# Performance work log

Hardware: AMD Instinct MI355X
Metric: run time of the kernel (lower is better)

The kernel has to match this reference:

```python
import jax, jax.numpy as jnp
import numpy as np
from jax import lax

IN_CH = 512
OUT_CH = 512
K = 3
W_DIM = 512
PAD = K // 2
EPS = 1e-8


def setup_inputs() -> dict:
    key = jax.random.key(0)
    k1, k2, k3, k4 = jax.random.split(key, 4)
    B, H, W = 8, 64, 64
    x = jax.random.normal(k1, (B, IN_CH, H, W), dtype=jnp.float32)
    w = jax.random.normal(k2, (B, W_DIM), dtype=jnp.float32)
    weight = jax.random.normal(k3, (OUT_CH, IN_CH, K, K), dtype=jnp.float32)
    bias = jnp.zeros((OUT_CH,), dtype=jnp.float32)
    # nn.Linear(512, in_ch): weight [in_ch, 512], bias [in_ch]
    lim = 1.0 / np.sqrt(W_DIM)
    affine_w = jax.random.uniform(k4, (IN_CH, W_DIM), dtype=jnp.float32, minval=-lim, maxval=lim)
    affine_b = jnp.zeros((IN_CH,), dtype=jnp.float32)
    return {"x": x, "w": w, "weight": weight, "bias": bias,
            "affine_w": affine_w, "affine_b": affine_b}


def _conv_one(xi, wi):
    # xi: [C, H, W], wi: [O, C, K, K] -> [O, H, W]
    out = lax.conv_general_dilated(
        xi[None], wi, window_strides=(1, 1),
        padding=[(PAD, PAD), (PAD, PAD)],
        dimension_numbers=("NCHW", "OIHW", "NCHW"))
    return out[0]


def reference(x, w, weight, bias, affine_w, affine_b):
    # style: [B, C] -> broadcast as [B, 1, C, 1, 1]
    style = w @ affine_w.T + affine_b
    wmod = weight[None] * (style[:, None, :, None, None] + 1.0)  # [B, O, C, K, K]
    # demodulate
    sigma = lax.rsqrt(jnp.sum(wmod * wmod, axis=(2, 3, 4), keepdims=True) + EPS)
    wmod = wmod * sigma
    # per-sample conv (equivalent to groups=B grouped conv)
    out = jax.vmap(_conv_one)(x, wmod)  # [B, O, H, W]
    return out + bias[None, :, None, None]
```

## Files before the change

kernel.cpp:

```cpp
#include <hip/hip_runtime.h>
#include <hip/hip_bf16.h>

typedef __attribute__((ext_vector_type(8))) short bf16x8;
typedef __attribute__((ext_vector_type(4))) float f32x4;

#define FSW(c) (((c) >> 1) & 3)

static __device__ __forceinline__ uint bf16rne(float f) {
    uint u = __float_as_uint(f);
    return (u + 0x7fffu + ((u >> 16) & 1u)) >> 16;
}

__global__ void k_style(const float* __restrict__ w, const float* __restrict__ aw,
                        const float* __restrict__ ab, float* __restrict__ style) {
    int idx = blockIdx.x * 4 + (threadIdx.x >> 6);
    int lane = threadIdx.x & 63;
    int b = idx >> 9, c = idx & 511;
    const float* wp = w + b * 512;
    const float* ap = aw + (size_t)c * 512;
    float s = 0.f;
    #pragma unroll
    for (int i = 0; i < 8; ++i) s += wp[lane + i * 64] * ap[lane + i * 64];
    #pragma unroll
    for (int m = 32; m; m >>= 1) s += __shfl_xor(s, m, 64);
    if (lane == 0) style[idx] = s + ab[c] + 1.0f;
}

__global__ void k_wprep(const float* __restrict__ weight, ushort* __restrict__ Wf,
                        float* __restrict__ wsq) {
    int t = blockIdx.x * 256 + threadIdx.x;
    int o = t >> 9, c = t & 511;
    int grp = o >> 5, rr = o & 31, fm = rr >> 4, l15r = rr & 15;
    int chunkid = c >> 5, kgw = (c >> 3) & 3, kk = c & 7;
    int lanew = kgw * 16 + l15r;
    const float* wp = weight + (size_t)t * 9;
    size_t G = (size_t)(grp * 16 + chunkid);
    size_t base = G * 9216 + (size_t)fm * 512 + (size_t)lanew * 8 + kk;
    float sq = 0.f;
    #pragma unroll
    for (int j = 0; j < 9; ++j) {
        float v = wp[j];
        sq += v * v;
        Wf[base + (size_t)j * 1024] = (ushort)bf16rne(v);
    }
    wsq[t] = sq;
}

__global__ void k_sigma(const float* __restrict__ style, const float* __restrict__ wsq,
                        float* __restrict__ sigma) {
    int idx = blockIdx.x * 4 + (threadIdx.x >> 6);
    int lane = threadIdx.x & 63;
    int b = idx >> 9, o = idx & 511;
    const float* sp = style + b * 512;
    const float* qp = wsq + (size_t)o * 512;
    float s = 0.f;
    #pragma unroll
    for (int i = 0; i < 8; ++i) {
        float st = sp[lane + i * 64];
        s += st * st * qp[lane + i * 64];
    }
    #pragma unroll
    for (int m = 32; m; m >>= 1) s += __shfl_xor(s, m, 64);
    if (lane == 0) sigma[idx] = rsqrtf(s + 1e-8f);
}

__global__ void k_premod(const float* __restrict__ x, const float* __restrict__ style,
                         ushort* __restrict__ xb) {
    int bid = blockIdx.x;
    int b = bid >> 6, y = bid & 63;
    int xcol = threadIdx.x >> 2, cg = threadIdx.x & 3;
    const float* sp = style + b * 512;
    #pragma unroll 1
    for (int cb = 0; cb < 16; ++cb) {
        int c0 = cb * 32 + cg * 8;
        float v[8];
        #pragma unroll
        for (int j = 0; j < 8; ++j)
            v[j] = x[((size_t)(b * 512 + c0 + j) * 64 + y) * 64 + xcol] * sp[c0 + j];
        uint4 pk;
        pk.x = bf16rne(v[0]) | (bf16rne(v[1]) << 16);
        pk.y = bf16rne(v[2]) | (bf16rne(v[3]) << 16);
        pk.z = bf16rne(v[4]) | (bf16rne(v[5]) << 16);
        pk.w = bf16rne(v[6]) | (bf16rne(v[7]) << 16);
        *(uint4*)&xb[((size_t)(b * 64 + y) * 64 + xcol) * 512 + c0] = pk;
    }
}

#define ALOAD(ARR, G, CC) { \
    const ushort* Wc_ = Wbase + (size_t)(CC) * 9216 + (G) * 3072; \
    _Pragma("unroll") for (int q_ = 0; q_ < 6; ++q_) \
        ARR[q_] = *(const uint4*)(Wc_ + q_ * 512); }

#define MM(AV, BV, FM, FN) \
    acc[FM][FN] = __builtin_amdgcn_mfma_f32_16x16x32_bf16( \
        *(const bf16x8*)&(AV), (BV), acc[FM][FN], 0, 0, 0)

#define HGROUP(AARR, H) \
    _Pragma("unroll") for (int dx_ = 0; dx_ < 3; ++dx_) { \
      _Pragma("unroll") for (int q_ = 0; q_ < 4; ++q_) { \
        MM(AARR[dx_ * 2 + 0], bv[dx_ * 4 + q_], 0, (H) * 4 + q_); \
        MM(AARR[dx_ * 2 + 1], bv[dx_ * 4 + q_], 1, (H) * 4 + q_); \
      } }

#define ROW(R, MFMAS) { \
    bf16x8 bv[12]; \
    _Pragma("unroll") for (int dx_ = 0; dx_ < 3; ++dx_) { \
      _Pragma("unroll") for (int q_ = 0; q_ < 4; ++q_) { \
        int ci_ = dx_ + q_ * 16 + l15; \
        bv[dx_ * 4 + q_] = *(const bf16x8*)&sX[cur][((R) * 66 + ci_) * 32 + ((kg ^ FSW(ci_)) * 8)]; \
      } } \
    __builtin_amdgcn_s_setprio(1); \
    MFMAS \
    __builtin_amdgcn_s_setprio(0); }

__global__ __launch_bounds__(256, 2) void k_conv(
    const ushort* __restrict__ xb, const ushort* __restrict__ Wf,
    const float* __restrict__ sigma, const float* __restrict__ bias,
    float* __restrict__ out) {

    __shared__ ushort sX[2][4 * 66 * 32];

    const int tid = threadIdx.x, bid = blockIdx.x;
    const int ob = bid & 3, pb = bid >> 2;
    const int b = pb >> 5, y0 = (pb & 31) * 2;
    const int o0 = ob * 128;
    const int wv = tid >> 6, lane = tid & 63;
    const int l15 = lane & 15, kg = lane >> 4;

    const int scol = (tid >> 2) & 63;
    const int skg = tid & 3;
    const int colpos = scol + 1;
    const int sslot = (skg ^ FSW(colpos)) * 8;
    const ushort* xrow_base = xb + ((size_t)(b * 64) * 64 + scol) * 512 + skg * 8;

    const int grp = ob * 4 + wv;
    const ushort* Wbase = Wf + (size_t)grp * 147456 + lane * 8;

    f32x4 acc[2][8];
    #pragma unroll
    for (int i = 0; i < 2; ++i)
        #pragma unroll
        for (int j = 0; j < 8; ++j) acc[i][j] = (f32x4){0.f, 0.f, 0.f, 0.f};

    if (tid < 64) {
        int buf = tid >> 5, rem = tid & 31;
        int r = rem >> 3, side = (rem >> 2) & 1, sl = rem & 3;
        int cp = side * 65;
        *(uint4*)&sX[buf][(r * 66 + cp) * 32 + sl * 8] = make_uint4(0u, 0u, 0u, 0u);
    }

    uint4 xs[4];
    #pragma unroll
    for (int p = 0; p < 4; ++p) {
        int yy = y0 - 1 + p;
        xs[p] = ((unsigned)yy < 64u)
              ? *(const uint4*)(xrow_base + (size_t)yy * 32768)
              : make_uint4(0u, 0u, 0u, 0u);
    }
    #pragma unroll
    for (int p = 0; p < 4; ++p)
        *(uint4*)&sX[0][(p * 66 + colpos) * 32 + sslot] = xs[p];

    uint4 a0[6], a1[6], a2[6];
    ALOAD(a0, 0, 0); ALOAD(a1, 1, 0); ALOAD(a2, 2, 0);
    __syncthreads();

    int cur = 0;
    #pragma unroll 1
    for (int cci = 0; cci < 16; ++cci) {
        const int ncc = (cci + 1) & 15;

        #pragma unroll
        for (int p = 0; p < 4; ++p) {
            int yy = y0 - 1 + p;
            xs[p] = ((unsigned)yy < 64u)
                  ? *(const uint4*)(xrow_base + (size_t)yy * 32768 + ncc * 32)
                  : make_uint4(0u, 0u, 0u, 0u);
        }

        ROW(0, HGROUP(a0, 0))
        ROW(1, HGROUP(a0, 1) HGROUP(a1, 0))
        ALOAD(a0, 0, ncc);
        ROW(2, HGROUP(a1, 1) HGROUP(a2, 0))
        ALOAD(a1, 1, ncc);
        ROW(3, HGROUP(a2, 1))
        ALOAD(a2, 2, ncc);

        #pragma unroll
        for (int p = 0; p < 4; ++p)
            *(uint4*)&sX[cur ^ 1][(p * 66 + colpos) * 32 + sslot] = xs[p];
        __syncthreads();
        cur ^= 1;
    }

    const float* sigb = sigma + b * 512;
    #pragma unroll
    for (int fm = 0; fm < 2; ++fm) {
        #pragma unroll
        for (int j = 0; j < 4; ++j) {
            int o = o0 + wv * 32 + fm * 16 + kg * 4 + j;
            float sg = sigb[o];
            float bs = bias[o];
            float* op = out + ((size_t)(b * 512 + o) * 64 + y0) * 64;
            #pragma unroll
            for (int fn = 0; fn < 8; ++fn)
                op[(fn >> 2) * 64 + (fn & 3) * 16 + l15] = acc[fm][fn][j] * sg + bs;
        }
    }
}

extern "C" void kernel_launch(void* const* d_in, const int* in_sizes, int n_in,
                              void* d_out, int out_size, void* d_ws, size_t ws_size,
                              hipStream_t stream) {
    const float* x    = (const float*)d_in[0];
    const float* w    = (const float*)d_in[1];
    const float* wt   = (const float*)d_in[2];
    const float* bias = (const float*)d_in[3];
    const float* aw   = (const float*)d_in[4];
    const float* ab   = (const float*)d_in[5];
    float* out = (float*)d_out;

    float* style  = (float*)d_ws;
    float* sigmap = style + 4096;
    float* wsq    = sigmap + 4096;
    ushort* Wf    = (ushort*)(wsq + 512 * 512);
    ushort* xbm   = Wf + 2359296;

    k_style <<<1024, 256, 0, stream>>>(w, aw, ab, style);
    k_wprep <<<1024, 256, 0, stream>>>(wt, Wf, wsq);
    k_premod<<< 512, 256, 0, stream>>>(x, style, xbm);
    k_sigma <<<1024, 256, 0, stream>>>(style, wsq, sigmap);
    k_conv  <<<1024, 256, 0, stream>>>(xbm, Wf, sigmap, bias, out);
}
```

Before: 150.5 us.

## Fuse input style modulation and bf16 packing into conv kernel, drop premod pass

Removes the separate premod kernel that wrote a channel-last bf16 copy of the style-scaled input. The conv kernel now has each wave read 32 fp32 channels of one input row directly from NCHW x, multiply by style, convert to bf16 and write into the swizzled shared tile. The next-chunk load and pack are interleaved between MFMA rows, and the third weight prefetch is moved after the barrier. This cuts one kernel launch and a full write plus read of the intermediate tensor. In exchange the conv reads fp32 data (twice the bytes), each input row is re-read by the neighbouring row-pair blocks and by all four output blocks, and register pressure rises by 32 floats.

After: 156.1 us. 1.04x slower.

```diff
diff --git a/kernel.cpp b/kernel.cpp
--- a/kernel.cpp
+++ b/kernel.cpp
@@ -64,32 +64,10 @@
     if (lane == 0) sigma[idx] = rsqrtf(s + 1e-8f);
 }
 
-__global__ void k_premod(const float* __restrict__ x, const float* __restrict__ style,
-                         ushort* __restrict__ xb) {
-    int bid = blockIdx.x;
-    int b = bid >> 6, y = bid & 63;
-    int xcol = threadIdx.x >> 2, cg = threadIdx.x & 3;
-    const float* sp = style + b * 512;
-    #pragma unroll 1
-    for (int cb = 0; cb < 16; ++cb) {
-        int c0 = cb * 32 + cg * 8;
-        float v[8];
-        #pragma unroll
-        for (int j = 0; j < 8; ++j)
-            v[j] = x[((size_t)(b * 512 + c0 + j) * 64 + y) * 64 + xcol] * sp[c0 + j];
-        uint4 pk;
-        pk.x = bf16rne(v[0]) | (bf16rne(v[1]) << 16);
-        pk.y = bf16rne(v[2]) | (bf16rne(v[3]) << 16);
-        pk.z = bf16rne(v[4]) | (bf16rne(v[5]) << 16);
-        pk.w = bf16rne(v[6]) | (bf16rne(v[7]) << 16);
-        *(uint4*)&xb[((size_t)(b * 64 + y) * 64 + xcol) * 512 + c0] = pk;
-    }
-}
-
-#define ALOAD(ARR, G, CC) { \
-    const ushort* Wc_ = Wbase + (size_t)(CC) * 9216 + (G) * 3072; \
+#define ALOAD(SL, DY, CC) { \
+    const ushort* p_ = Wbase + (size_t)(CC) * 9216 + (DY) * 3072; \
     _Pragma("unroll") for (int q_ = 0; q_ < 6; ++q_) \
-        ARR[q_] = *(const uint4*)(Wc_ + q_ * 512); }
+        SL[q_] = *(const uint4*)(p_ + q_ * 512); }
 
 #define MM(AV, BV, FM, FN) \
     acc[FM][FN] = __builtin_amdgcn_mfma_f32_16x16x32_bf16( \
@@ -104,19 +82,30 @@
 
 #define ROW(R, MFMAS) { \
     bf16x8 bv[12]; \
-    _Pragma("unroll") for (int dx_ = 0; dx_ < 3; ++dx_) { \
-      _Pragma("unroll") for (int q_ = 0; q_ < 4; ++q_) { \
+    _Pragma("unroll") for (int dx_ = 0; dx_ < 3; ++dx_) \
+    _Pragma("unroll") for (int q_ = 0; q_ < 4; ++q_) { \
         int ci_ = dx_ + q_ * 16 + l15; \
         bv[dx_ * 4 + q_] = *(const bf16x8*)&sX[cur][((R) * 66 + ci_) * 32 + ((kg ^ FSW(ci_)) * 8)]; \
-      } } \
+    } \
     __builtin_amdgcn_s_setprio(1); \
     MFMAS \
     __builtin_amdgcn_s_setprio(0); }
 
+#define XPACK_WRITE(BUF) { \
+    ushort* dst_ = &sX[BUF][(wv * 66 + colpos) * 32]; \
+    _Pragma("unroll") for (int g_ = 0; g_ < 4; ++g_) { \
+        uint4 pk_; \
+        pk_.x = bf16rne(xv[g_*8+0]) | (bf16rne(xv[g_*8+1]) << 16); \
+        pk_.y = bf16rne(xv[g_*8+2]) | (bf16rne(xv[g_*8+3]) << 16); \
+        pk_.z = bf16rne(xv[g_*8+4]) | (bf16rne(xv[g_*8+5]) << 16); \
+        pk_.w = bf16rne(xv[g_*8+6]) | (bf16rne(xv[g_*8+7]) << 16); \
+        *(uint4*)&dst_[(g_ ^ FSW(colpos)) * 8] = pk_; \
+    } }
+
 __global__ __launch_bounds__(256, 2) void k_conv(
-    const ushort* __restrict__ xb, const ushort* __restrict__ Wf,
-    const float* __restrict__ sigma, const float* __restrict__ bias,
-    float* __restrict__ out) {
+    const float* __restrict__ x, const ushort* __restrict__ Wf,
+    const float* __restrict__ style, const float* __restrict__ sigma,
+    const float* __restrict__ bias, float* __restrict__ out) {
 
     __shared__ ushort sX[2][4 * 66 * 32];
 
@@ -127,11 +116,12 @@
     const int wv = tid >> 6, lane = tid & 63;
     const int l15 = lane & 15, kg = lane >> 4;
 
-    const int scol = (tid >> 2) & 63;
-    const int skg = tid & 3;
+    const int scol = lane;
+    const int yy = y0 - 1 + wv;
+    const bool yok = (unsigned)yy < 64u;
     const int colpos = scol + 1;
-    const int sslot = (skg ^ FSW(colpos)) * 8;
-    const ushort* xrow_base = xb + ((size_t)(b * 64) * 64 + scol) * 512 + skg * 8;
+    const float* xcb = x + (((size_t)(b * 512) * 64 + yy) * 64 + scol);
+    const float* stb = style + b * 512;
 
     const int grp = ob * 4 + wv;
     const ushort* Wbase = Wf + (size_t)grp * 147456 + lane * 8;
@@ -149,20 +139,18 @@
         *(uint4*)&sX[buf][(r * 66 + cp) * 32 + sl * 8] = make_uint4(0u, 0u, 0u, 0u);
     }
 
-    uint4 xs[4];
-    #pragma unroll
-    for (int p = 0; p < 4; ++p) {
-        int yy = y0 - 1 + p;
-        xs[p] = ((unsigned)yy < 64u)
-              ? *(const uint4*)(xrow_base + (size_t)yy * 32768)
-              : make_uint4(0u, 0u, 0u, 0u);
-    }
-    #pragma unroll
-    for (int p = 0; p < 4; ++p)
-        *(uint4*)&sX[0][(p * 66 + colpos) * 32 + sslot] = xs[p];
+    float xv[32];
+    if (yok) {
+        #pragma unroll
+        for (int j = 0; j < 32; ++j) xv[j] = xcb[(size_t)j * 4096] * stb[j];
+    } else {
+        #pragma unroll
+        for (int j = 0; j < 32; ++j) xv[j] = 0.f;
+    }
+    XPACK_WRITE(0)
 
     uint4 a0[6], a1[6], a2[6];
-    ALOAD(a0, 0, 0); ALOAD(a1, 1, 0); ALOAD(a2, 2, 0);
+    ALOAD(a0, 0, 0) ALOAD(a1, 1, 0) ALOAD(a2, 2, 0)
     __syncthreads();
 
     int cur = 0;
@@ -170,27 +158,26 @@
     for (int cci = 0; cci < 16; ++cci) {
         const int ncc = (cci + 1) & 15;
 
-        #pragma unroll
-        for (int p = 0; p < 4; ++p) {
-            int yy = y0 - 1 + p;
-            xs[p] = ((unsigned)yy < 64u)
-                  ? *(const uint4*)(xrow_base + (size_t)yy * 32768 + ncc * 32)
-                  : make_uint4(0u, 0u, 0u, 0u);
+        ROW(0, HGROUP(a0, 0))
+
+        if (yok) {
+            #pragma unroll
+            for (int j = 0; j < 32; ++j)
+                xv[j] = xcb[(size_t)(ncc * 32 + j) * 4096] * stb[ncc * 32 + j];
         }
 
-        ROW(0, HGROUP(a0, 0))
         ROW(1, HGROUP(a0, 1) HGROUP(a1, 0))
-        ALOAD(a0, 0, ncc);
+        ALOAD(a0, 0, ncc)
+
+        XPACK_WRITE(cur ^ 1)
+
         ROW(2, HGROUP(a1, 1) HGROUP(a2, 0))
-        ALOAD(a1, 1, ncc);
+        ALOAD(a1, 1, ncc)
         ROW(3, HGROUP(a2, 1))
-        ALOAD(a2, 2, ncc);
-
-        #pragma unroll
-        for (int p = 0; p < 4; ++p)
-            *(uint4*)&sX[cur ^ 1][(p * 66 + colpos) * 32 + sslot] = xs[p];
+
         __syncthreads();
         cur ^= 1;
+        ALOAD(a2, 2, ncc)
     }
 
     const float* sigb = sigma + b * 512;
@@ -224,11 +211,9 @@
     float* sigmap = style + 4096;
     float* wsq    = sigmap + 4096;
     ushort* Wf    = (ushort*)(wsq + 512 * 512);
-    ushort* xbm   = Wf + 2359296;
-
-    k_style <<<1024, 256, 0, stream>>>(w, aw, ab, style);
-    k_wprep <<<1024, 256, 0, stream>>>(wt, Wf, wsq);
-    k_premod<<< 512, 256, 0, stream>>>(x, style, xbm);
-    k_sigma <<<1024, 256, 0, stream>>>(style, wsq, sigmap);
-    k_conv  <<<1024, 256, 0, stream>>>(xbm, Wf, sigmap, bias, out);
-}
+
+    k_style<<<1024, 256, 0, stream>>>(w, aw, ab, style);
+    k_wprep<<<1024, 256, 0, stream>>>(wt, Wf, wsq);
+    k_sigma<<<1024, 256, 0, stream>>>(style, wsq, sigmap);
+    k_conv <<<1024, 256, 0, stream>>>(x, Wf, style, sigmap, bias, out);
+}
```

## Merge prep kernels into two launches and remap conv block order

Applied to the files above, without the earlier changes.

Combines style/weight-prep and sigma/premodulation kernels into two launches with block-range dispatch, removing launch gaps. The conv kernel's block index is remapped so blocks sharing an output-channel group are scheduled together, with pixel blocks interleaved across batches, to change cache reuse of weights versus activations. The last weight-fragment load is moved after the barrier to shift register pressure and overlap. The remap may reduce reuse of activation tiles across output groups.

Result: faster. 142.4 us (-5.4%).

```diff
diff --git a/kernel.cpp b/kernel.cpp
--- a/kernel.cpp
+++ b/kernel.cpp
@@ -11,85 +11,86 @@
     return (u + 0x7fffu + ((u >> 16) & 1u)) >> 16;
 }
 
-__global__ void k_style(const float* __restrict__ w, const float* __restrict__ aw,
-                        const float* __restrict__ ab, float* __restrict__ style) {
-    int idx = blockIdx.x * 4 + (threadIdx.x >> 6);
-    int lane = threadIdx.x & 63;
-    int b = idx >> 9, c = idx & 511;
-    const float* wp = w + b * 512;
-    const float* ap = aw + (size_t)c * 512;
-    float s = 0.f;
-    #pragma unroll
-    for (int i = 0; i < 8; ++i) s += wp[lane + i * 64] * ap[lane + i * 64];
-    #pragma unroll
-    for (int m = 32; m; m >>= 1) s += __shfl_xor(s, m, 64);
-    if (lane == 0) style[idx] = s + ab[c] + 1.0f;
-}
-
-__global__ void k_wprep(const float* __restrict__ weight, ushort* __restrict__ Wf,
-                        float* __restrict__ wsq) {
-    int t = blockIdx.x * 256 + threadIdx.x;
-    int o = t >> 9, c = t & 511;
-    int grp = o >> 5, rr = o & 31, fm = rr >> 4, l15r = rr & 15;
-    int chunkid = c >> 5, kgw = (c >> 3) & 3, kk = c & 7;
-    int lanew = kgw * 16 + l15r;
-    const float* wp = weight + (size_t)t * 9;
-    size_t G = (size_t)(grp * 16 + chunkid);
-    size_t base = G * 9216 + (size_t)fm * 512 + (size_t)lanew * 8 + kk;
-    float sq = 0.f;
-    #pragma unroll
-    for (int j = 0; j < 9; ++j) {
-        float v = wp[j];
-        sq += v * v;
-        Wf[base + (size_t)j * 1024] = (ushort)bf16rne(v);
-    }
-    wsq[t] = sq;
-}
-
-__global__ void k_sigma(const float* __restrict__ style, const float* __restrict__ wsq,
-                        float* __restrict__ sigma) {
-    int idx = blockIdx.x * 4 + (threadIdx.x >> 6);
-    int lane = threadIdx.x & 63;
-    int b = idx >> 9, o = idx & 511;
-    const float* sp = style + b * 512;
-    const float* qp = wsq + (size_t)o * 512;
-    float s = 0.f;
-    #pragma unroll
-    for (int i = 0; i < 8; ++i) {
-        float st = sp[lane + i * 64];
-        s += st * st * qp[lane + i * 64];
-    }
-    #pragma unroll
-    for (int m = 32; m; m >>= 1) s += __shfl_xor(s, m, 64);
-    if (lane == 0) sigma[idx] = rsqrtf(s + 1e-8f);
-}
-
-__global__ void k_premod(const float* __restrict__ x, const float* __restrict__ style,
-                         ushort* __restrict__ xb) {
-    int bid = blockIdx.x;
-    int b = bid >> 6, y = bid & 63;
-    int xcol = threadIdx.x >> 2, cg = threadIdx.x & 3;
-    const float* sp = style + b * 512;
-    #pragma unroll 1
-    for (int cb = 0; cb < 16; ++cb) {
-        int c0 = cb * 32 + cg * 8;
-        float v[8];
-        #pragma unroll
-        for (int j = 0; j < 8; ++j)
-            v[j] = x[((size_t)(b * 512 + c0 + j) * 64 + y) * 64 + xcol] * sp[c0 + j];
-        uint4 pk;
-        pk.x = bf16rne(v[0]) | (bf16rne(v[1]) << 16);
-        pk.y = bf16rne(v[2]) | (bf16rne(v[3]) << 16);
-        pk.z = bf16rne(v[4]) | (bf16rne(v[5]) << 16);
-        pk.w = bf16rne(v[6]) | (bf16rne(v[7]) << 16);
-        *(uint4*)&xb[((size_t)(b * 64 + y) * 64 + xcol) * 512 + c0] = pk;
-    }
-}
-
-#define ALOAD(ARR, G, CC) { \
-    const ushort* Wc_ = Wbase + (size_t)(CC) * 9216 + (G) * 3072; \
+__global__ void k_prep1(const float* __restrict__ weight, ushort* __restrict__ Wf,
+                        float* __restrict__ wsq, const float* __restrict__ w,
+                        const float* __restrict__ aw, const float* __restrict__ ab,
+                        float* __restrict__ style) {
+    if (blockIdx.x < 1024) {
+        int t = blockIdx.x * 256 + threadIdx.x;
+        int o = t >> 9, c = t & 511;
+        int grp = o >> 5, rr = o & 31, fm = rr >> 4, l15r = rr & 15;
+        int chunkid = c >> 5, kgw = (c >> 3) & 3, kk = c & 7;
+        int lanew = kgw * 16 + l15r;
+        const float* wp = weight + (size_t)t * 9;
+        size_t G = (size_t)(grp * 16 + chunkid);
+        size_t base = G * 9216 + (size_t)fm * 512 + (size_t)lanew * 8 + kk;
+        float sq = 0.f;
+        #pragma unroll
+        for (int j = 0; j < 9; ++j) {
+            float v = wp[j];
+            sq += v * v;
+            Wf[base + (size_t)j * 1024] = (ushort)bf16rne(v);
+        }
+        wsq[t] = sq;
+    } else {
+        int idx = (blockIdx.x - 1024) * 4 + (threadIdx.x >> 6);
+        int lane = threadIdx.x & 63;
+        int b = idx >> 9, c = idx & 511;
+        const float* wp = w + b * 512;
+        const float* ap = aw + (size_t)c * 512;
+        float s = 0.f;
+        #pragma unroll
+        for (int i = 0; i < 8; ++i) s += wp[lane + i * 64] * ap[lane + i * 64];
+        #pragma unroll
+        for (int m = 32; m; m >>= 1) s += __shfl_xor(s, m, 64);
+        if (lane == 0) style[idx] = s + ab[c] + 1.0f;
+    }
+}
+
+__global__ void k_prep2(const float* __restrict__ style, const float* __restrict__ wsq,
+                        float* __restrict__ sigma, const float* __restrict__ x,
+                        ushort* __restrict__ xb) {
+    if (blockIdx.x < 1024) {
+        int idx = blockIdx.x * 4 + (threadIdx.x >> 6);
+        int lane = threadIdx.x & 63;
+        int b = idx >> 9, o = idx & 511;
+        const float* sp = style + b * 512;
+        const float* qp = wsq + (size_t)o * 512;
+        float s = 0.f;
+        #pragma unroll
+        for (int i = 0; i < 8; ++i) {
+            float st = sp[lane + i * 64];
+            s += st * st * qp[lane + i * 64];
+        }
+        #pragma unroll
+        for (int m = 32; m; m >>= 1) s += __shfl_xor(s, m, 64);
+        if (lane == 0) sigma[idx] = rsqrtf(s + 1e-8f);
+    } else {
+        int bid = blockIdx.x - 1024;
+        int b = bid >> 6, y = bid & 63;
+        int xcol = threadIdx.x >> 2, cg = threadIdx.x & 3;
+        const float* sp = style + b * 512;
+        #pragma unroll 1
+        for (int cb = 0; cb < 16; ++cb) {
+            int c0 = cb * 32 + cg * 8;
+            float v[8];
+            #pragma unroll
+            for (int j = 0; j < 8; ++j)
+                v[j] = x[((size_t)(b * 512 + c0 + j) * 64 + y) * 64 + xcol] * sp[c0 + j];
+            uint4 pk;
+            pk.x = bf16rne(v[0]) | (bf16rne(v[1]) << 16);
+            pk.y = bf16rne(v[2]) | (bf16rne(v[3]) << 16);
+            pk.z = bf16rne(v[4]) | (bf16rne(v[5]) << 16);
+            pk.w = bf16rne(v[6]) | (bf16rne(v[7]) << 16);
+            *(uint4*)&xb[((size_t)(b * 64 + y) * 64 + xcol) * 512 + c0] = pk;
+        }
+    }
+}
+
+#define ALOAD(SL, DY, CC) { \
+    const ushort* p_ = Wbase + (size_t)(CC) * 9216 + (DY) * 3072; \
     _Pragma("unroll") for (int q_ = 0; q_ < 6; ++q_) \
-        ARR[q_] = *(const uint4*)(Wc_ + q_ * 512); }
+        SL[q_] = *(const uint4*)(p_ + q_ * 512); }
 
 #define MM(AV, BV, FM, FN) \
     acc[FM][FN] = __builtin_amdgcn_mfma_f32_16x16x32_bf16( \
@@ -104,11 +105,11 @@
 
 #define ROW(R, MFMAS) { \
     bf16x8 bv[12]; \
-    _Pragma("unroll") for (int dx_ = 0; dx_ < 3; ++dx_) { \
-      _Pragma("unroll") for (int q_ = 0; q_ < 4; ++q_) { \
+    _Pragma("unroll") for (int dx_ = 0; dx_ < 3; ++dx_) \
+    _Pragma("unroll") for (int q_ = 0; q_ < 4; ++q_) { \
         int ci_ = dx_ + q_ * 16 + l15; \
         bv[dx_ * 4 + q_] = *(const bf16x8*)&sX[cur][((R) * 66 + ci_) * 32 + ((kg ^ FSW(ci_)) * 8)]; \
-      } } \
+    } \
     __builtin_amdgcn_s_setprio(1); \
     MFMAS \
     __builtin_amdgcn_s_setprio(0); }
@@ -121,7 +122,8 @@
     __shared__ ushort sX[2][4 * 66 * 32];
 
     const int tid = threadIdx.x, bid = blockIdx.x;
-    const int ob = bid & 3, pb = bid >> 2;
+    const int ob = bid >> 8;
+    const int pb = ((bid & 7) << 5) | ((bid >> 3) & 31);
     const int b = pb >> 5, y0 = (pb & 31) * 2;
     const int o0 = ob * 128;
     const int wv = tid >> 6, lane = tid & 63;
@@ -162,7 +164,7 @@
         *(uint4*)&sX[0][(p * 66 + colpos) * 32 + sslot] = xs[p];
 
     uint4 a0[6], a1[6], a2[6];
-    ALOAD(a0, 0, 0); ALOAD(a1, 1, 0); ALOAD(a2, 2, 0);
+    ALOAD(a0, 0, 0) ALOAD(a1, 1, 0) ALOAD(a2, 2, 0)
     __syncthreads();
 
     int cur = 0;
@@ -180,17 +182,17 @@
 
         ROW(0, HGROUP(a0, 0))
         ROW(1, HGROUP(a0, 1) HGROUP(a1, 0))
-        ALOAD(a0, 0, ncc);
+        ALOAD(a0, 0, ncc)
         ROW(2, HGROUP(a1, 1) HGROUP(a2, 0))
-        ALOAD(a1, 1, ncc);
+        ALOAD(a1, 1, ncc)
         ROW(3, HGROUP(a2, 1))
-        ALOAD(a2, 2, ncc);
 
         #pragma unroll
         for (int p = 0; p < 4; ++p)
             *(uint4*)&sX[cur ^ 1][(p * 66 + colpos) * 32 + sslot] = xs[p];
         __syncthreads();
         cur ^= 1;
+        ALOAD(a2, 2, ncc)
     }
 
     const float* sigb = sigma + b * 512;
@@ -226,9 +228,7 @@
     ushort* Wf    = (ushort*)(wsq + 512 * 512);
     ushort* xbm   = Wf + 2359296;
 
-    k_style <<<1024, 256, 0, stream>>>(w, aw, ab, style);
-    k_wprep <<<1024, 256, 0, stream>>>(wt, Wf, wsq);
-    k_premod<<< 512, 256, 0, stream>>>(x, style, xbm);
-    k_sigma <<<1024, 256, 0, stream>>>(style, wsq, sigmap);
-    k_conv  <<<1024, 256, 0, stream>>>(xbm, Wf, sigmap, bias, out);
-}
+    k_prep1<<<2048, 256, 0, stream>>>(wt, Wf, wsq, w, aw, ab, style);
+    k_prep2<<<1536, 256, 0, stream>>>(style, wsq, sigmap, x, xbm);
+    k_conv <<<1024, 256, 0, stream>>>(xbm, Wf, sigmap, bias, out);
+}
```
